# Kernel tuning notes

Measured on AMD Instinct MI355X. Metric: run time of the kernel, lower is better.

Reference implementation:

```python
import jax, jax.numpy as jnp
import numpy as np
import math

B, S, E = 4, 2048, 1024


def setup_inputs() -> dict:
    key = jax.random.key(0)
    ks = jax.random.split(key, 7)
    w_scale = 1.0 / math.sqrt(E)
    x = jax.random.normal(ks[0], (B, S, E), dtype=jnp.float32)
    Wq = jax.random.normal(ks[1], (E, E), dtype=jnp.float32) * w_scale
    bq = jax.random.normal(ks[2], (E,), dtype=jnp.float32) * 0.01
    Wk = jax.random.normal(ks[3], (E, E), dtype=jnp.float32) * w_scale
    bk = jax.random.normal(ks[4], (E,), dtype=jnp.float32) * 0.01
    Wv = jax.random.normal(ks[5], (E, E), dtype=jnp.float32) * w_scale
    bv = jax.random.normal(ks[6], (E,), dtype=jnp.float32) * 0.01
    # causal mask: True = attend, False = masked (mask == 0 -> -inf)
    mask = jnp.broadcast_to(jnp.tril(jnp.ones((S, S), dtype=bool)), (B, S, S))
    return {"x": x, "Wq": Wq, "bq": bq, "Wk": Wk, "bk": bk, "Wv": Wv, "bv": bv, "mask": mask}


def reference(x, Wq, bq, Wk, bk, Wv, bv, mask):
    # nn.Linear stores weight as [out, in]: y = x @ W.T + b
    Q = jnp.einsum("bse,oe->bso", x, Wq) + bq
    K = jnp.einsum("bse,oe->bso", x, Wk) + bk
    V = jnp.einsum("bse,oe->bso", x, Wv) + bv
    scale = math.sqrt(E)
    scores = jnp.einsum("bqe,bke->bqk", Q, K) / scale  # [B,S,S]
    scores = jnp.where(mask, scores, -jnp.inf)
    attn = jax.nn.softmax(scores, axis=-1)
    out = jnp.einsum("bqk,bke->bqe", attn, V)  # [B,S,E]
    return out
```

## Files before the change

### kernel.cpp

```cpp
#include <hip/hip_runtime.h>
#include <stdint.h>

typedef unsigned short u16;
typedef __attribute__((ext_vector_type(8))) short bf16x8;
typedef __attribute__((ext_vector_type(4))) float f32x4;

#define MFMA16(a, b, c) __builtin_amdgcn_mfma_f32_16x16x32_bf16((a), (b), (c), 0, 0, 0)

#define MASKVAL (-1.0e30f)

#define WAITV(N) asm volatile("s_waitcnt vmcnt(" #N ")" ::: "memory")
#define LGKM0()  asm volatile("s_waitcnt lgkmcnt(0)" ::: "memory")
#define SBAR()   __builtin_amdgcn_s_barrier()

__device__ __forceinline__ u16 f2bf(float f) {
  union { float f; uint32_t u; } v; v.f = f;
  uint32_t u = v.u;
  u += 0x7fffu + ((u >> 16) & 1u);
  return (u16)(u >> 16);
}
__device__ __forceinline__ void async16(const void* g, void* l) {
  __builtin_amdgcn_global_load_lds(
      (const __attribute__((address_space(1))) unsigned int*)g,
      (__attribute__((address_space(3))) unsigned int*)l, 16, 0, 0);
}

__global__ __launch_bounds__(256) void conv_kernel(
    const float* __restrict__ x,  const float* __restrict__ wq,
    const float* __restrict__ wk, const float* __restrict__ wv,
    u16* __restrict__ xb, u16* __restrict__ wb, int do_wv)
{
  const int NX = 1 << 20;
  const int NW = 1 << 17;
  const int total = NX + NW * (do_wv ? 3 : 2);
  for (int i = blockIdx.x * 256 + threadIdx.x; i < total; i += gridDim.x * 256) {
    const float* src; u16* dst;
    if (i < NX) {
      src = x + (size_t)i * 8;
      const int m = i >> 7, k8 = i & 127;
      dst = xb + (size_t)m * 2048 + 1024 + k8 * 8;
    } else {
      const int j = i - NX;
      const int wsel = j >> 17;
      const int jj = j & (NW - 1);
      const float* W = (wsel == 0) ? wq : (wsel == 1) ? wk : wv;
      const int zoff = (wsel == 0) ? 0 : (wsel == 1) ? (2 << 20) : (1 << 20);
      src = W + (size_t)jj * 8;
      dst = wb + zoff + jj * 8;
    }
    float4 f0 = *(const float4*)src;
    float4 f1 = *(const float4*)(src + 4);
    ushort4 h0, h1;
    h0.x = f2bf(f0.x); h0.y = f2bf(f0.y); h0.z = f2bf(f0.z); h0.w = f2bf(f0.w);
    h1.x = f2bf(f1.x); h1.y = f2bf(f1.y); h1.z = f2bf(f1.z); h1.w = f2bf(f1.w);
    *(ushort4*)dst = h0;
    *(ushort4*)(dst + 4) = h1;
  }
}

template <int BMODE>
__global__ __launch_bounds__(256) void gemm_kernel(
    const u16* __restrict__ xb,
    const u16* __restrict__ wb,
    const float* __restrict__ wv_f,
    const float* __restrict__ bq, const float* __restrict__ bk,
    const float* __restrict__ bv,
    u16* __restrict__ q_out, u16* __restrict__ vt_out, u16* __restrict__ k_out,
    int mode)
{
  __shared__ u16 lA[2][128 * 32];
  __shared__ u16 lB[2][128 * 32];

  const int flat = blockIdx.x;
  const int xcd = flat & 7, idx = flat >> 3;
  int n_g, mm, z;
  if (mode == 0)      { n_g = xcd * 3 + idx % 3;  mm = idx / 3;  z = n_g >> 3; }
  else if (mode == 1) { n_g = xcd * 2 + (idx & 1); mm = idx >> 1; z = (n_g < 8) ? 0 : 2; }
  else                { n_g = xcd;                 mm = idx;      z = 1; }
  const int m0 = mm * 128, n0 = (n_g & 7) * 128;

  const int tid = threadIdx.x, lane = tid & 63, w = tid >> 6;
  const int quad = lane >> 4, l15 = lane & 15;
  const int wr = (w >> 1) * 64, wc = (w & 1) * 64;

  const u16* wz = wb + ((size_t)z << 20);
  const float* bias = (z == 0) ? bq : (z == 1) ? bv : bk;

  const int sr  = lane >> 2;
  const int ssw = (lane >> 3) & 3;
  const int c16s = (lane & 3) ^ ssw;

  auto stageA = [&](int kk, int bbuf) {
    const int k0 = kk * 32;
#pragma unroll
    for (int i = 0; i < 2; ++i) {
      const int r = w * 32 + i * 16 + sr;
      async16(&xb[(size_t)(m0 + r) * 2048 + 1024 + k0 + c16s * 8],
              &lA[bbuf][w * 1024 + i * 512]);
    }
  };
  auto stageB = [&](int kk, int bbuf) {
    const int k0 = kk * 32;
#pragma unroll
    for (int i = 0; i < 2; ++i) {
      const int r = w * 32 + i * 16 + sr;
      async16(&wz[(size_t)(n0 + r) * 1024 + k0 + c16s * 8],
              &lB[bbuf][w * 1024 + i * 512]);
    }
  };

  float4 bfr[4];
  const int br = tid >> 1;
  const int bcb = (tid & 1) * 2;
  const int bs = (br >> 1) & 3;
  auto loadB = [&](int kk) {
    const float* p = &wv_f[(size_t)(n0 + br) * 1024 + kk * 32 + bcb * 8];
    bfr[0] = ((const float4*)p)[0];
    bfr[1] = ((const float4*)p)[1];
    bfr[2] = ((const float4*)p)[2];
    bfr[3] = ((const float4*)p)[3];
  };
  auto writeB = [&](int bbuf) {
    ushort4 h[4];
#pragma unroll
    for (int g = 0; g < 4; ++g) {
      h[g].x = f2bf(bfr[g].x); h[g].y = f2bf(bfr[g].y);
      h[g].z = f2bf(bfr[g].z); h[g].w = f2bf(bfr[g].w);
    }
    const int p0 = (bcb + 0) ^ bs, p1 = (bcb + 1) ^ bs;
    *(ushort4*)&lB[bbuf][br * 32 + p0 * 8]     = h[0];
    *(ushort4*)&lB[bbuf][br * 32 + p0 * 8 + 4] = h[1];
    *(ushort4*)&lB[bbuf][br * 32 + p1 * 8]     = h[2];
    *(ushort4*)&lB[bbuf][br * 32 + p1 * 8 + 4] = h[3];
  };

  f32x4 zero4 = {0.f, 0.f, 0.f, 0.f};
  f32x4 acc[4][4];
#pragma unroll
  for (int i = 0; i < 4; ++i)
#pragma unroll
    for (int j = 0; j < 4; ++j) acc[i][j] = zero4;

  if constexpr (BMODE == 0) {
    stageA(0, 0); stageB(0, 0);
  } else {
    stageA(0, 0); loadB(0); writeB(0);
  }

  const int fxor = (l15 >> 1) & 3;
  for (int kk = 0; kk < 32; ++kk) {
    const int bbuf = kk & 1;
    __syncthreads();
    if (kk + 1 < 32) {
      stageA(kk + 1, bbuf ^ 1);
      if constexpr (BMODE == 0) stageB(kk + 1, bbuf ^ 1);
      else loadB(kk + 1);
    }
    bf16x8 af[4], bw[4];
#pragma unroll
    for (int mf = 0; mf < 4; ++mf)
      af[mf] = *(const bf16x8*)
          &lA[bbuf][(wr + mf * 16 + l15) * 32 + (quad ^ fxor) * 8];
#pragma unroll
    for (int nf = 0; nf < 4; ++nf)
      bw[nf] = *(const bf16x8*)
          &lB[bbuf][(wc + nf * 16 + l15) * 32 + (quad ^ fxor) * 8];
    __builtin_amdgcn_s_setprio(1);
#pragma unroll
    for (int mf = 0; mf < 4; ++mf)
#pragma unroll
      for (int nf = 0; nf < 4; ++nf)
        acc[mf][nf] = MFMA16(af[mf], bw[nf], acc[mf][nf]);
    __builtin_amdgcn_s_setprio(0);
    if constexpr (BMODE == 1) {
      if (kk + 1 < 32) writeB(bbuf ^ 1);
    }
  }

  float bvv[4];
#pragma unroll
  for (int nf = 0; nf < 4; ++nf)
    bvv[nf] = bias[n0 + wc + nf * 16 + l15];

  if (z == 0) {
    const float qs = 0.03125f;
#pragma unroll
    for (int mf = 0; mf < 4; ++mf) {
#pragma unroll
      for (int nf = 0; nf < 4; ++nf) {
        const int n = n0 + wc + nf * 16 + l15;
#pragma unroll
        for (int r = 0; r < 4; ++r) {
          const int m = m0 + wr + mf * 16 + quad * 4 + r;
          q_out[(size_t)m * 2048 + n] = f2bf((acc[mf][nf][r] + bvv[nf]) * qs);
        }
      }
    }
  } else if (z == 1) {
#pragma unroll
    for (int mf = 0; mf < 4; ++mf) {
      const int mbase = m0 + wr + mf * 16 + quad * 4;
      const int bb = mbase >> 11;
      const int ss = mbase & 2047;
#pragma unroll
      for (int nf = 0; nf < 4; ++nf) {
        const int n = n0 + wc + nf * 16 + l15;
        ushort4 pk;
        pk.x = f2bf(acc[mf][nf][0] + bvv[nf]);
        pk.y = f2bf(acc[mf][nf][1] + bvv[nf]);
        pk.z = f2bf(acc[mf][nf][2] + bvv[nf]);
        pk.w = f2bf(acc[mf][nf][3] + bvv[nf]);
        *(ushort4*)&vt_out[((size_t)bb << 21) + (size_t)n * 2048 + ss] = pk;
      }
    }
  } else {
#pragma unroll
    for (int mf = 0; mf < 4; ++mf) {
#pragma unroll
      for (int nf = 0; nf < 4; ++nf) {
        const int n = n0 + wc + nf * 16 + l15;
#pragma unroll
        for (int r = 0; r < 4; ++r) {
          const int m = m0 + wr + mf * 16 + quad * 4 + r;
          k_out[(size_t)m * 1024 + n] = f2bf(acc[mf][nf][r] + bvv[nf]);
        }
      }
    }
  }
}

__global__ __launch_bounds__(512) void attn_kernel(
    const u16* __restrict__ Q, const u16* __restrict__ K,
    const u16* __restrict__ VT, float* out)
{
  constexpr int SLOT = 20480;
  __shared__ u16   ring[3][SLOT];
  __shared__ float sS[32 * 132];
  __shared__ u16   sP[32 * 136];
  __shared__ float sAlpha[32];
  __shared__ float sLinv[32];

  const int lin = blockIdx.x + ((int)blockIdx.y << 6);
  const int xcd = lin & 7;
  const int t = ((lin >> 3) << 1) | (xcd & 1);
  const int b = xcd >> 1;
  const int q0 = t * 32;
  const int tid = threadIdx.x, lane = tid & 63, w = tid >> 6;
  const int quad = lane >> 4, l15 = lane & 15;
  const u16* Qb  = Q  + ((size_t)b << 22);
  const u16* Kb  = K  + ((size_t)b << 21);
  const u16* VTb = VT + ((size_t)b << 21);
  float* outb = out + ((size_t)b << 21);

  const int sr = lane >> 4;
  const int sp = lane & 15;

  auto issueK = [&](int kv0, int e0, u16* slot) {
#pragma unroll
    for (int jj = 0; jj < 4; ++jj) {
      const int j = w * 4 + jj;
      const int r = j * 4 + sr;
      const int c16 = sp ^ (r & 15);
      async16(&Kb[(size_t)(kv0 + r) * 1024 + e0 + c16 * 8], slot + j * 512);
    }
  };
  auto issueV = [&](int kv0, int ck, u16* slot) {
#pragma unroll
    for (int jj = 0; jj < 4; ++jj) {
      const int j = w * 4 + jj;
      const int r = j * 4 + sr;
      const int c16 = sp ^ (r & 15);
      async16(&VTb[(size_t)(ck * 128 + r) * 2048 + kv0 + c16 * 8], slot + j * 512);
    }
  };
  auto issueQ = [&](int cq, u16* slot) {
    const int r = w * 4 + sr;
    const int c16 = sp ^ (r & 15);
    async16(&Qb[(size_t)(q0 + r) * 2048 + cq * 128 + c16 * 8],
            slot + 16384 + w * 512);
  };

  f32x4 zero4 = {0.f, 0.f, 0.f, 0.f};
  f32x4 accO[8][2];
#pragma unroll
  for (int c = 0; c < 8; ++c)
#pragma unroll
    for (int i = 0; i < 2; ++i) accO[c][i] = zero4;

  float m_i = MASKVAL, l_i = 0.f;
  const int srow = tid >> 4, slane = tid & 15;

  issueK(0, 0, ring[0]);   issueQ(0, ring[0]);
  issueK(0, 128, ring[1]); issueQ(1, ring[1]);
  int sl = 0, sl2 = 2;

  const int niter = q0 / 128 + 1;
  for (int it = 0; it < niter; ++it) {
    const int kv0 = it * 128;

    f32x4 accS[2];
    accS[0] = zero4; accS[1] = zero4;

#pragma unroll
    for (int c = 0; c < 8; ++c) {
      if (c < 7) { WAITV(5); } else { WAITV(4); }
      SBAR();
      u16* dst = ring[sl2];
      if (c < 6)      { issueK(kv0, (c + 2) * 128, dst); issueQ(c + 2, dst); }
      else if (c == 6) issueV(kv0, 0, dst);
      else             issueV(kv0, 1, dst);
      const u16* bufK = ring[sl];
      const u16* bufQ = ring[sl] + 16384;
      __builtin_amdgcn_s_setprio(1);
#pragma unroll
      for (int ks = 0; ks < 4; ++ks) {
        const int cc = ks * 4 + quad;
        bf16x8 a0 = *(const bf16x8*)&bufQ[l15 * 128 + (cc ^ l15) * 8];
        bf16x8 a1 = *(const bf16x8*)&bufQ[(16 + l15) * 128 + (cc ^ l15) * 8];
        bf16x8 b0 = *(const bf16x8*)&bufK[(w * 16 + l15) * 128 + (cc ^ l15) * 8];
        accS[0] = MFMA16(a0, b0, accS[0]);
        accS[1] = MFMA16(a1, b0, accS[1]);
      }
      __builtin_amdgcn_s_setprio(0);
      sl  = (sl  == 2) ? 0 : sl  + 1;
      sl2 = (sl2 == 2) ? 0 : sl2 + 1;
    }

#pragma unroll
    for (int mf = 0; mf < 2; ++mf)
#pragma unroll
      for (int r = 0; r < 4; ++r) {
        const int row = mf * 16 + quad * 4 + r;
        const int col = w * 16 + l15;
        sS[row * 132 + col] = (kv0 + col <= q0 + row) ? accS[mf][r] : MASKVAL;
      }
    LGKM0();
    SBAR();

    {
      float v[8];
      float4 t0 = *(const float4*)&sS[srow * 132 + slane * 8 + 0];
      float4 t1 = *(const float4*)&sS[srow * 132 + slane * 8 + 4];
      v[0]=t0.x; v[1]=t0.y; v[2]=t0.z; v[3]=t0.w;
      v[4]=t1.x; v[5]=t1.y; v[6]=t1.z; v[7]=t1.w;
      float mx = v[0];
#pragma unroll
      for (int j = 1; j < 8; ++j) mx = fmaxf(mx, v[j]);
#pragma unroll
      for (int d = 1; d < 16; d <<= 1) mx = fmaxf(mx, __shfl_xor(mx, d, 64));
      const float mnew  = fmaxf(m_i, mx);
      const float alpha = __expf(m_i - mnew);
      float sum = 0.f;
      u16 pb[8];
#pragma unroll
      for (int j = 0; j < 8; ++j) {
        const float p = __expf(v[j] - mnew);
        pb[j] = f2bf(p);
        union { uint32_t u; float f; } pv; pv.u = ((uint32_t)pb[j]) << 16;
        sum += pv.f;
      }
      ushort4 pk0, pk1;
      pk0.x = pb[0]; pk0.y = pb[1]; pk0.z = pb[2]; pk0.w = pb[3];
      pk1.x = pb[4]; pk1.y = pb[5]; pk1.z = pb[6]; pk1.w = pb[7];
      *(ushort4*)&sP[srow * 136 + slane * 8 + 0] = pk0;
      *(ushort4*)&sP[srow * 136 + slane * 8 + 4] = pk1;
#pragma unroll
      for (int d = 1; d < 16; d <<= 1) sum += __shfl_xor(sum, d, 64);
      l_i = l_i * alpha + sum;
      m_i = mnew;
      if (slane == 0) sAlpha[srow] = alpha;
      if (it == niter - 1 && slane == 0) sLinv[srow] = 1.0f / l_i;
    }
    LGKM0();
    SBAR();

    float av[2][4];
#pragma unroll
    for (int mf = 0; mf < 2; ++mf)
#pragma unroll
      for (int r = 0; r < 4; ++r)
        av[mf][r] = sAlpha[mf * 16 + quad * 4 + r];
#pragma unroll
    for (int c = 0; c < 8; ++c)
#pragma unroll
      for (int mf = 0; mf < 2; ++mf)
#pragma unroll
        for (int r = 0; r < 4; ++r) accO[c][mf][r] *= av[mf][r];

    bf16x8 pf0[4], pf1[4];
#pragma unroll
    for (int ks = 0; ks < 4; ++ks) {
      const int cc = ks * 4 + quad;
      pf0[ks] = *(const bf16x8*)&sP[l15 * 136 + cc * 8];
      pf1[ks] = *(const bf16x8*)&sP[(16 + l15) * 136 + cc * 8];
    }

#pragma unroll
    for (int k = 0; k < 8; ++k) {
      if (k < 7)                 { WAITV(4); }
      else if (it + 1 < niter)   { WAITV(5); }
      else                       { WAITV(0); }
      SBAR();
      u16* dst = ring[sl2];
      if (k < 6) issueV(kv0, k + 2, dst);
      else if (it + 1 < niter) {
        issueK(kv0 + 128, (k - 6) * 128, dst);
        issueQ(k - 6, dst);
      }
      const u16* bufV = ring[sl];
      __builtin_amdgcn_s_setprio(1);
#pragma unroll
      for (int ks = 0; ks < 4; ++ks) {
        const int cc = ks * 4 + quad;
        bf16x8 v0 = *(const bf16x8*)&bufV[(w * 16 + l15) * 128 + (cc ^ l15) * 8];
        accO[k][0] = MFMA16(pf0[ks], v0, accO[k][0]);
        accO[k][1] = MFMA16(pf1[ks], v0, accO[k][1]);
      }
      __builtin_amdgcn_s_setprio(0);
      sl  = (sl  == 2) ? 0 : sl  + 1;
      sl2 = (sl2 == 2) ? 0 : sl2 + 1;
    }
  }

  float lv[2][4];
#pragma unroll
  for (int mf = 0; mf < 2; ++mf)
#pragma unroll
    for (int r = 0; r < 4; ++r)
      lv[mf][r] = sLinv[mf * 16 + quad * 4 + r];
#pragma unroll
  for (int c = 0; c < 8; ++c)
#pragma unroll
    for (int mf = 0; mf < 2; ++mf) {
      const int col = c * 128 + w * 16 + l15;
#pragma unroll
      for (int r = 0; r < 4; ++r) {
        const int row = q0 + mf * 16 + quad * 4 + r;
        outb[(size_t)row * 1024 + col] = accO[c][mf][r] * lv[mf][r];
      }
    }
}

extern "C" void kernel_launch(void* const* d_in, const int* in_sizes, int n_in,
                              void* d_out, int out_size, void* d_ws, size_t ws_size,
                              hipStream_t stream) {
  (void)in_sizes; (void)n_in; (void)out_size;
  const float* x  = (const float*)d_in[0];
  const float* Wq = (const float*)d_in[1];
  const float* bq = (const float*)d_in[2];
  const float* Wk = (const float*)d_in[3];
  const float* bk = (const float*)d_in[4];
  const float* Wv = (const float*)d_in[5];
  const float* bv = (const float*)d_in[6];

  u16* qbuf = (u16*)d_out;
  u16* vtw  = (u16*)d_in[7];
  u16* kw   = (u16*)d_ws;

  const bool ws_big = ws_size >= (size_t)22 * 1024 * 1024;
  u16* wb = ws_big ? (u16*)d_ws + (8u << 20) : (u16*)d_in[7];

  conv_kernel<<<dim3(2048), 256, 0, stream>>>(x, Wq, Wk, Wv, qbuf, wb,
                                              ws_big ? 1 : 0);
  if (ws_big) {
    gemm_kernel<0><<<dim3(1536), 256, 0, stream>>>(
        qbuf, wb, Wv, bq, bk, bv, qbuf, vtw, kw, 0);
  } else {
    gemm_kernel<0><<<dim3(1024), 256, 0, stream>>>(
        qbuf, wb, Wv, bq, bk, bv, qbuf, vtw, kw, 1);
    gemm_kernel<1><<<dim3(512), 256, 0, stream>>>(
        qbuf, wb, Wv, bq, bk, bv, qbuf, vtw, kw, 2);
  }

  attn_kernel<<<dim3(64, 4), 512, 0, stream>>>(qbuf, kw, vtw, (float*)d_out);
}
```

Before: 414.0 us.

## Triple-buffer GEMM with vmcnt waits and always use fused single GEMM launch

```diff
diff --git a/kernel.cpp b/kernel.cpp
--- a/kernel.cpp
+++ b/kernel.cpp
@@ -25,29 +25,36 @@
       (__attribute__((address_space(3))) unsigned int*)l, 16, 0, 0);
 }
 
-__global__ __launch_bounds__(256) void conv_kernel(
-    const float* __restrict__ x,  const float* __restrict__ wq,
-    const float* __restrict__ wk, const float* __restrict__ wv,
-    u16* __restrict__ xb, u16* __restrict__ wb, int do_wv)
+__global__ __launch_bounds__(256) void conv1_kernel(
+    const float* __restrict__ x, u16* __restrict__ xbI)
 {
   const int NX = 1 << 20;
+  for (int i = blockIdx.x * 256 + threadIdx.x; i < NX; i += gridDim.x * 256) {
+    const float* src = x + (size_t)i * 8;
+    const int m = i >> 7, k8 = i & 127;
+    float4 f0 = *(const float4*)src;
+    float4 f1 = *(const float4*)(src + 4);
+    ushort4 h0, h1;
+    h0.x = f2bf(f0.x); h0.y = f2bf(f0.y); h0.z = f2bf(f0.z); h0.w = f2bf(f0.w);
+    h1.x = f2bf(f1.x); h1.y = f2bf(f1.y); h1.z = f2bf(f1.z); h1.w = f2bf(f1.w);
+    u16* dI = xbI + (size_t)m * 2048 + 1024 + k8 * 8;
+    *(ushort4*)dI = h0; *(ushort4*)(dI + 4) = h1;
+  }
+}
+
+__global__ __launch_bounds__(256) void conv2_kernel(
+    const float* __restrict__ wq, const float* __restrict__ wk,
+    const float* __restrict__ wv, u16* __restrict__ wb)
+{
   const int NW = 1 << 17;
-  const int total = NX + NW * (do_wv ? 3 : 2);
-  for (int i = blockIdx.x * 256 + threadIdx.x; i < total; i += gridDim.x * 256) {
-    const float* src; u16* dst;
-    if (i < NX) {
-      src = x + (size_t)i * 8;
-      const int m = i >> 7, k8 = i & 127;
-      dst = xb + (size_t)m * 2048 + 1024 + k8 * 8;
-    } else {
-      const int j = i - NX;
-      const int wsel = j >> 17;
-      const int jj = j & (NW - 1);
-      const float* W = (wsel == 0) ? wq : (wsel == 1) ? wk : wv;
-      const int zoff = (wsel == 0) ? 0 : (wsel == 1) ? (2 << 20) : (1 << 20);
-      src = W + (size_t)jj * 8;
-      dst = wb + zoff + jj * 8;
-    }
+  const int total = NW * 3;
+  for (int j = blockIdx.x * 256 + threadIdx.x; j < total; j += gridDim.x * 256) {
+    const int wsel = j >> 17;
+    const int jj = j & (NW - 1);
+    const float* W = (wsel == 0) ? wq : (wsel == 1) ? wk : wv;
+    const int zoff = (wsel == 0) ? 0 : (wsel == 1) ? (2 << 20) : (1 << 20);
+    const float* src = W + (size_t)jj * 8;
+    u16* dst = wb + zoff + jj * 8;
     float4 f0 = *(const float4*)src;
     float4 f1 = *(const float4*)(src + 4);
     ushort4 h0, h1;
@@ -58,25 +65,21 @@
   }
 }
 
-template <int BMODE>
 __global__ __launch_bounds__(256) void gemm_kernel(
     const u16* __restrict__ xb,
     const u16* __restrict__ wb,
-    const float* __restrict__ wv_f,
     const float* __restrict__ bq, const float* __restrict__ bk,
     const float* __restrict__ bv,
-    u16* __restrict__ q_out, u16* __restrict__ vt_out, u16* __restrict__ k_out,
-    int mode)
+    u16* __restrict__ q_out, u16* __restrict__ vt_out, u16* __restrict__ k_out)
 {
-  __shared__ u16 lA[2][128 * 32];
-  __shared__ u16 lB[2][128 * 32];
+  __shared__ u16 lA[3][128 * 32];
+  __shared__ u16 lB[3][128 * 32];
 
   const int flat = blockIdx.x;
   const int xcd = flat & 7, idx = flat >> 3;
-  int n_g, mm, z;
-  if (mode == 0)      { n_g = xcd * 3 + idx % 3;  mm = idx / 3;  z = n_g >> 3; }
-  else if (mode == 1) { n_g = xcd * 2 + (idx & 1); mm = idx >> 1; z = (n_g < 8) ? 0 : 2; }
-  else                { n_g = xcd;                 mm = idx;      z = 1; }
+  const int n_g = xcd * 3 + idx % 3;
+  const int mm  = idx / 3;
+  const int z   = n_g >> 3;
   const int m0 = mm * 128, n0 = (n_g & 7) * 128;
 
   const int tid = threadIdx.x, lane = tid & 63, w = tid >> 6;
@@ -109,31 +112,6 @@
     }
   };
 
-  float4 bfr[4];
-  const int br = tid >> 1;
-  const int bcb = (tid & 1) * 2;
-  const int bs = (br >> 1) & 3;
-  auto loadB = [&](int kk) {
-    const float* p = &wv_f[(size_t)(n0 + br) * 1024 + kk * 32 + bcb * 8];
-    bfr[0] = ((const float4*)p)[0];
-    bfr[1] = ((const float4*)p)[1];
-    bfr[2] = ((const float4*)p)[2];
-    bfr[3] = ((const float4*)p)[3];
-  };
-  auto writeB = [&](int bbuf) {
-    ushort4 h[4];
-#pragma unroll
-    for (int g = 0; g < 4; ++g) {
-      h[g].x = f2bf(bfr[g].x); h[g].y = f2bf(bfr[g].y);
-      h[g].z = f2bf(bfr[g].z); h[g].w = f2bf(bfr[g].w);
-    }
-    const int p0 = (bcb + 0) ^ bs, p1 = (bcb + 1) ^ bs;
-    *(ushort4*)&lB[bbuf][br * 32 + p0 * 8]     = h[0];
-    *(ushort4*)&lB[bbuf][br * 32 + p0 * 8 + 4] = h[1];
-    *(ushort4*)&lB[bbuf][br * 32 + p1 * 8]     = h[2];
-    *(ushort4*)&lB[bbuf][br * 32 + p1 * 8 + 4] = h[3];
-  };
-
   f32x4 zero4 = {0.f, 0.f, 0.f, 0.f};
   f32x4 acc[4][4];
 #pragma unroll
@@ -141,30 +119,28 @@
 #pragma unroll
     for (int j = 0; j < 4; ++j) acc[i][j] = zero4;
 
-  if constexpr (BMODE == 0) {
-    stageA(0, 0); stageB(0, 0);
-  } else {
-    stageA(0, 0); loadB(0); writeB(0);
-  }
+  stageA(0, 0); stageB(0, 0);
+  stageA(1, 1); stageB(1, 1);
 
   const int fxor = (l15 >> 1) & 3;
+  int cur = 0;
   for (int kk = 0; kk < 32; ++kk) {
-    const int bbuf = kk & 1;
-    __syncthreads();
-    if (kk + 1 < 32) {
-      stageA(kk + 1, bbuf ^ 1);
-      if constexpr (BMODE == 0) stageB(kk + 1, bbuf ^ 1);
-      else loadB(kk + 1);
+    if (kk < 31) { WAITV(4); } else { WAITV(0); }
+    SBAR();
+    if (kk + 2 < 32) {
+      int nx = cur + 2; if (nx >= 3) nx -= 3;
+      stageA(kk + 2, nx);
+      stageB(kk + 2, nx);
     }
     bf16x8 af[4], bw[4];
 #pragma unroll
     for (int mf = 0; mf < 4; ++mf)
       af[mf] = *(const bf16x8*)
-          &lA[bbuf][(wr + mf * 16 + l15) * 32 + (quad ^ fxor) * 8];
+          &lA[cur][(wr + mf * 16 + l15) * 32 + (quad ^ fxor) * 8];
 #pragma unroll
     for (int nf = 0; nf < 4; ++nf)
       bw[nf] = *(const bf16x8*)
-          &lB[bbuf][(wc + nf * 16 + l15) * 32 + (quad ^ fxor) * 8];
+          &lB[cur][(wc + nf * 16 + l15) * 32 + (quad ^ fxor) * 8];
     __builtin_amdgcn_s_setprio(1);
 #pragma unroll
     for (int mf = 0; mf < 4; ++mf)
@@ -172,9 +148,7 @@
       for (int nf = 0; nf < 4; ++nf)
         acc[mf][nf] = MFMA16(af[mf], bw[nf], acc[mf][nf]);
     __builtin_amdgcn_s_setprio(0);
-    if constexpr (BMODE == 1) {
-      if (kk + 1 < 32) writeB(bbuf ^ 1);
-    }
+    cur = (cur == 2) ? 0 : cur + 1;
   }
 
   float bvv[4];
@@ -444,7 +418,7 @@
 extern "C" void kernel_launch(void* const* d_in, const int* in_sizes, int n_in,
                               void* d_out, int out_size, void* d_ws, size_t ws_size,
                               hipStream_t stream) {
-  (void)in_sizes; (void)n_in; (void)out_size;
+  (void)in_sizes; (void)n_in; (void)out_size; (void)ws_size;
   const float* x  = (const float*)d_in[0];
   const float* Wq = (const float*)d_in[1];
   const float* bq = (const float*)d_in[2];
@@ -456,21 +430,11 @@
   u16* qbuf = (u16*)d_out;
   u16* vtw  = (u16*)d_in[7];
   u16* kw   = (u16*)d_ws;
-
-  const bool ws_big = ws_size >= (size_t)22 * 1024 * 1024;
-  u16* wb = ws_big ? (u16*)d_ws + (8u << 20) : (u16*)d_in[7];
-
-  conv_kernel<<<dim3(2048), 256, 0, stream>>>(x, Wq, Wk, Wv, qbuf, wb,
-                                              ws_big ? 1 : 0);
-  if (ws_big) {
-    gemm_kernel<0><<<dim3(1536), 256, 0, stream>>>(
-        qbuf, wb, Wv, bq, bk, bv, qbuf, vtw, kw, 0);
-  } else {
-    gemm_kernel<0><<<dim3(1024), 256, 0, stream>>>(
-        qbuf, wb, Wv, bq, bk, bv, qbuf, vtw, kw, 1);
-    gemm_kernel<1><<<dim3(512), 256, 0, stream>>>(
-        qbuf, wb, Wv, bq, bk, bv, qbuf, vtw, kw, 2);
-  }
-
+  u16* wb   = (u16*)d_in[0];
+
+  conv1_kernel<<<dim3(2048), 256, 0, stream>>>(x, qbuf);
+  conv2_kernel<<<dim3(512), 256, 0, stream>>>(Wq, Wk, Wv, wb);
+  gemm_kernel<<<dim3(1536), 256, 0, stream>>>(qbuf, wb, bq, bk, bv,
+                                              qbuf, vtw, kw);
   attn_kernel<<<dim3(64, 4), 512, 0, stream>>>(qbuf, kw, vtw, (float*)d_out);
 }
```

Result: no change. 417.5 us (+0.8%).
